# Kernel optimization log

Hardware: AMD Instinct MI355X
Metric: run time of the kernel (lower is better)

## Reference

```python
import jax, jax.numpy as jnp
import numpy as np

B_SZ, SEQ, D_MODEL, D_STATE = 4, 4096, 1024, 16
LN_EPS = 1e-5


def setup_inputs() -> dict:
    key = jax.random.key(0)
    ks = jax.random.split(key, 6)
    x = jax.random.normal(ks[0], (B_SZ, SEQ, D_MODEL), jnp.float32)
    # A_log ~ U(-3, -1) per _init_weights
    A_log = jax.random.uniform(ks[1], (D_MODEL, D_STATE), jnp.float32, -3.0, -1.0)
    # xavier-ish init for projections
    B_w = jax.random.normal(ks[2], (D_STATE, D_MODEL), jnp.float32) / np.sqrt(D_MODEL)
    C_w = jax.random.normal(ks[3], (D_STATE, D_MODEL), jnp.float32) / np.sqrt(D_MODEL)
    D = jnp.ones((D_MODEL,), jnp.float32)
    gate_w = jax.random.normal(ks[4], (D_MODEL, D_MODEL), jnp.float32) / np.sqrt(D_MODEL)
    gate_b = jnp.zeros((D_MODEL,), jnp.float32)
    ln_gamma = jnp.ones((D_MODEL,), jnp.float32)
    ln_beta = jnp.zeros((D_MODEL,), jnp.float32)
    return {"x": x, "A_log": A_log, "B_w": B_w, "C_w": C_w, "D": D,
            "gate_w": gate_w, "gate_b": gate_b,
            "ln_gamma": ln_gamma, "ln_beta": ln_beta}


def reference(x, A_log, B_w, C_w, D, gate_w, gate_b, ln_gamma, ln_beta):
    b, s, d = x.shape
    n = A_log.shape[1]
    A = jnp.exp(A_log)                      # [d, n]
    Bx = jnp.einsum('bsd,nd->bsn', x, B_w)  # input-dependent B_t
    Cx = jnp.einsum('bsd,nd->bsn', x, C_w)  # input-dependent C_t

    def step(h, inp):
        x_t, B_t, C_t = inp                 # [b,d], [b,n], [b,n]
        h = h * A[None] + B_t[:, None, :] * x_t[:, :, None]   # [b,d,n]
        y_t = jnp.einsum('bdn,bn->bd', h, C_t) + D * x_t
        return h, y_t

    h0 = jnp.zeros((b, d, n), x.dtype)
    xs = (jnp.swapaxes(x, 0, 1), jnp.swapaxes(Bx, 0, 1), jnp.swapaxes(Cx, 0, 1))
    _, ys = jax.lax.scan(step, h0, xs)      # ys: [s,b,d]
    y = jnp.swapaxes(ys, 0, 1)              # [b,s,d]

    gate = jax.nn.sigmoid(jnp.einsum('bsd,ed->bse', x, gate_w) + gate_b)
    out = gate * y + (1.0 - gate) * x

    mu = jnp.mean(out, axis=-1, keepdims=True)
    var = jnp.var(out, axis=-1, keepdims=True)
    out = (out - mu) * jax.lax.rsqrt(var + LN_EPS) * ln_gamma + ln_beta
    # dropout is identity in eval mode
    return out
```

## Files before the change

kernel.cpp:

```cpp
#include <hip/hip_runtime.h>

#define B_SZ 4
#define SEQ  4096
#define DM   1024
#define DSTATE 16
#define ROWS (B_SZ*SEQ)

typedef unsigned short u16;
typedef __attribute__((ext_vector_type(8))) short   s16x8;
typedef __attribute__((ext_vector_type(4))) float   f32x4;
typedef __attribute__((ext_vector_type(4))) u16     u16x4;

__device__ inline float bf2f(u16 u) {
    unsigned v = ((unsigned)u) << 16;
    float f; __builtin_memcpy(&f, &v, 4); return f;
}
__device__ inline u16 f2bf(float f) {
    unsigned u; __builtin_memcpy(&u, &f, 4);
    return (u16)((u + 0x7FFFu + ((u >> 16) & 1u)) >> 16);
}
__device__ inline f32x4 mfma16(s16x8 a, s16x8 b, f32x4 c) {
    return __builtin_amdgcn_mfma_f32_16x16x32_bf16(a, b, c, 0, 0, 0);
}
__device__ inline void gl_lds16(const u16* g, u16* l) {
    __builtin_amdgcn_global_load_lds(
        (const __attribute__((address_space(1))) unsigned int*)g,
        (__attribute__((address_space(3))) unsigned int*)l, 16, 0, 0);
}

__global__ __launch_bounds__(256) void k_cvt_w(
    const float* __restrict__ gw, const float* __restrict__ Bw,
    const float* __restrict__ Cw, u16* __restrict__ gwb,
    u16* __restrict__ bwh, u16* __restrict__ bwl,
    u16* __restrict__ cwh, u16* __restrict__ cwl)
{
    int blk = blockIdx.x;
    if (blk < 1024) {
        int i = blk * 256 + threadIdx.x;
        f32x4 v = ((const f32x4*)gw)[i];
        u16x4 o;
#pragma unroll
        for (int c = 0; c < 4; c++) o[c] = f2bf(v[c]);
        ((u16x4*)gwb)[i] = o;
    } else {
        int isC = (blk >= 1040);
        const float* src = isC ? Cw : Bw;
        u16* dh = isC ? cwh : bwh;
        u16* dl = isC ? cwl : bwl;
        int i = (blk - (isC ? 1040 : 1024)) * 256 + threadIdx.x;
        f32x4 v = ((const f32x4*)src)[i];
        u16x4 h, l;
#pragma unroll
        for (int c = 0; c < 4; c++) {
            h[c] = f2bf(v[c]);
            l[c] = f2bf(v[c] - bf2f(h[c]));
        }
        ((u16x4*)dh)[i] = h;
        ((u16x4*)dl)[i] = l;
    }
}

__global__ __launch_bounds__(64) void k_bxcx(
    const float* __restrict__ x,
    const u16* __restrict__ bwh, const u16* __restrict__ bwl,
    const u16* __restrict__ cwh, const u16* __restrict__ cwl,
    u16* __restrict__ xh,
    float* __restrict__ Bx, float* __restrict__ Cx)
{
    int lane = threadIdx.x;
    int lo = lane & 15, hi = lane >> 4;
    int m0 = blockIdx.x * 16;
    f32x4 accB = {}, accC = {};
    for (int k0 = 0; k0 < DM; k0 += 32) {
        size_t woff = (size_t)lo * DM + k0 + hi * 8;
        s16x8 bh = *(const s16x8*)(bwh + woff);
        s16x8 bl = *(const s16x8*)(bwl + woff);
        s16x8 ch = *(const s16x8*)(cwh + woff);
        s16x8 cl = *(const s16x8*)(cwl + woff);
        size_t aoff = (size_t)(m0 + lo) * DM + k0 + hi * 8;
        f32x4 v0 = *(const f32x4*)(x + aoff);
        f32x4 v1 = *(const f32x4*)(x + aoff + 4);
        s16x8 ah, al;
#pragma unroll
        for (int c = 0; c < 4; c++) {
            u16 h0 = f2bf(v0[c]);
            ah[c]     = (short)h0;
            al[c]     = (short)f2bf(v0[c] - bf2f(h0));
            u16 h1 = f2bf(v1[c]);
            ah[4 + c] = (short)h1;
            al[4 + c] = (short)f2bf(v1[c] - bf2f(h1));
        }
        *(s16x8*)(xh + aoff) = ah;
        accB = mfma16(ah, bh, accB);
        accB = mfma16(al, bh, accB);
        accB = mfma16(ah, bl, accB);
        accC = mfma16(ah, ch, accC);
        accC = mfma16(al, ch, accC);
        accC = mfma16(ah, cl, accC);
    }
#pragma unroll
    for (int r = 0; r < 4; r++) {
        int m = m0 + hi * 4 + r;
        Bx[(size_t)m * DSTATE + lo] = accB[r];
        Cx[(size_t)m * DSTATE + lo] = accC[r];
    }
}

#define GBM 256
#define GBN 256
#define GBK 64

__global__ __launch_bounds__(512) void k_gate(
    const u16* __restrict__ xh, const u16* __restrict__ gwb,
    const float* __restrict__ gb, float* __restrict__ gate)
{
    __shared__ u16 sA[2][GBM * GBK];
    __shared__ u16 sB[2][GBN * GBK];
    int tid = threadIdx.x;
    int wv = tid >> 6, lane = tid & 63;
    int lo = lane & 15, hi = lane >> 4;
    int wm = wv >> 2, wn = wv & 3;
    int m0 = blockIdx.x * GBM;
    int n0 = blockIdx.y * GBN;

    int r_in = lane >> 3;
    int p    = lane & 7;
    int c    = p ^ r_in;

    auto stage = [&](int buf, int k0) {
#pragma unroll
        for (int q = 0; q < 4; q++) {
            int r = q * 64 + wv * 8 + r_in;
            size_t goff = (size_t)r * DM + k0 + c * 8;
            gl_lds16(xh  + (size_t)m0 * DM + goff, &sA[buf][(q * 64 + wv * 8) * GBK]);
            gl_lds16(gwb + (size_t)n0 * DM + goff, &sB[buf][(q * 64 + wv * 8) * GBK]);
        }
    };

    f32x4 acc[8][4] = {};

    stage(0, 0);
    asm volatile("s_waitcnt vmcnt(0)" ::: "memory");
    __syncthreads();

    for (int ks = 0; ks < DM / GBK; ks++) {
        int buf = ks & 1;
        if (ks + 1 < DM / GBK) stage(buf ^ 1, (ks + 1) * GBK);
#pragma unroll
        for (int kk = 0; kk < 2; kk++) {
            s16x8 afr[8], bfr[4];
#pragma unroll
            for (int j = 0; j < 4; j++) {
                int rb = wn * 64 + j * 16 + lo;
                int pc = (kk * 4 + hi) ^ (rb & 7);
                bfr[j] = *(const s16x8*)&sB[buf][rb * GBK + pc * 8];
            }
#pragma unroll
            for (int i = 0; i < 8; i++) {
                int ra = wm * 128 + i * 16 + lo;
                int pc = (kk * 4 + hi) ^ (ra & 7);
                afr[i] = *(const s16x8*)&sA[buf][ra * GBK + pc * 8];
            }
#pragma unroll
            for (int i = 0; i < 8; i++)
#pragma unroll
                for (int j = 0; j < 4; j++)
                    acc[i][j] = mfma16(afr[i], bfr[j], acc[i][j]);
        }
        asm volatile("s_waitcnt vmcnt(0)" ::: "memory");
        __syncthreads();
    }

#pragma unroll
    for (int i = 0; i < 8; i++)
#pragma unroll
        for (int r = 0; r < 4; r++) {
            int m = m0 + wm * 128 + i * 16 + hi * 4 + r;
#pragma unroll
            for (int j = 0; j < 4; j++) {
                int n = n0 + wn * 64 + j * 16 + lo;
                float v = acc[i][j][r] + gb[n];
                gate[(size_t)m * DM + n] = 1.0f / (1.0f + __expf(-v));
            }
        }
}

#define CHUNK_L 64
#define LOOKBACK 16

__global__ __launch_bounds__(256) void k_scan(
    const float* __restrict__ x, const float* __restrict__ A_log,
    const float* __restrict__ Bx, const float* __restrict__ Cx,
    const float* __restrict__ Dvec, float* gate_out)
{
    __shared__ float sBx[(CHUNK_L + LOOKBACK) * DSTATE];
    __shared__ float sCx[(CHUNK_L + LOOKBACK) * DSTATE];
    int d = blockIdx.x * 256 + threadIdx.x;
    int b = blockIdx.z;
    int t0 = blockIdx.y * CHUNK_L;
    int tstart = t0 - LOOKBACK; if (tstart < 0) tstart = 0;
    int lb = t0 - tstart;
    int T  = lb + CHUNK_L;
    int NB = T >> 3;
    int nv = T * (DSTATE / 4);

    const f32x4* gBg = (const f32x4*)(Bx + ((size_t)b * SEQ + tstart) * DSTATE);
    const f32x4* gCg = (const f32x4*)(Cx + ((size_t)b * SEQ + tstart) * DSTATE);
    for (int i = threadIdx.x; i < nv; i += 256) {
        ((f32x4*)sBx)[i] = gBg[i];
        ((f32x4*)sCx)[i] = gCg[i];
    }

    float A[DSTATE], h[DSTATE];
    const f32x4* ga = (const f32x4*)(A_log + (size_t)d * DSTATE);
#pragma unroll
    for (int q = 0; q < 4; q++) {
        f32x4 av = ga[q];
#pragma unroll
        for (int c = 0; c < 4; c++) {
            A[q * 4 + c] = expf(av[c]);
            h[q * 4 + c] = 0.0f;
        }
    }
    float Dd = Dvec[d];
    __syncthreads();

    const float* xp = x + ((size_t)b * SEQ + tstart) * DM + d;
    float* gp = gate_out + ((size_t)b * SEQ + t0) * DM + d;

    const f32x4* sB4 = (const f32x4*)sBx;
    const f32x4* sC4 = (const f32x4*)sCx;

    auto pf = [&](int bd, float (&xr)[8], float (&gr)[8]) {
        int base = bd * 8;
#pragma unroll
        for (int q = 0; q < 8; q++) xr[q] = xp[(size_t)(base + q) * DM];
        if (base >= lb) {
#pragma unroll
            for (int q = 0; q < 8; q++) gr[q] = gp[(size_t)(base + q - lb) * DM];
        }
    };

    auto body = [&](int bd, float (&xr)[8], float (&gr)[8]) {
        int base = bd * 8;
        if (base >= lb) {
            float* go = gp + (size_t)(base - lb) * DM;
#pragma unroll
            for (int q = 0; q < 8; q++) {
                int idx = base + q;
                float xv = xr[q], gv = gr[q];
                f32x4 vb0 = sB4[idx * 4 + 0], vb1 = sB4[idx * 4 + 1];
                f32x4 vb2 = sB4[idx * 4 + 2], vb3 = sB4[idx * 4 + 3];
                f32x4 vc0 = sC4[idx * 4 + 0], vc1 = sC4[idx * 4 + 1];
                f32x4 vc2 = sC4[idx * 4 + 2], vc3 = sC4[idx * 4 + 3];
                float y0 = 0.f, y1 = 0.f, y2 = 0.f, y3 = 0.f;
#pragma unroll
                for (int c = 0; c < 4; c++) {
                    h[c]      = h[c]      * A[c]      + vb0[c] * xv;  y0 += h[c]      * vc0[c];
                    h[4 + c]  = h[4 + c]  * A[4 + c]  + vb1[c] * xv;  y1 += h[4 + c]  * vc1[c];
                    h[8 + c]  = h[8 + c]  * A[8 + c]  + vb2[c] * xv;  y2 += h[8 + c]  * vc2[c];
                    h[12 + c] = h[12 + c] * A[12 + c] + vb3[c] * xv;  y3 += h[12 + c] * vc3[c];
                }
                float yv = ((y0 + y1) + (y2 + y3)) + Dd * xv;
                go[(size_t)q * DM] = gv * yv + (1.0f - gv) * xv;
            }
        } else {
#pragma unroll
            for (int q = 0; q < 8; q++) {
                int idx = base + q;
                float xv = xr[q];
                f32x4 vb0 = sB4[idx * 4 + 0], vb1 = sB4[idx * 4 + 1];
                f32x4 vb2 = sB4[idx * 4 + 2], vb3 = sB4[idx * 4 + 3];
#pragma unroll
                for (int c = 0; c < 4; c++) {
                    h[c]      = h[c]      * A[c]      + vb0[c] * xv;
                    h[4 + c]  = h[4 + c]  * A[4 + c]  + vb1[c] * xv;
                    h[8 + c]  = h[8 + c]  * A[8 + c]  + vb2[c] * xv;
                    h[12 + c] = h[12 + c] * A[12 + c] + vb3[c] * xv;
                }
            }
        }
    };

    float xA[8], gA[8], xB[8], gB8[8];
    pf(0, xA, gA);
    for (int bd = 0; bd < NB; bd += 2) {
        pf(bd + 1, xB, gB8);
        body(bd, xA, gA);
        if (bd + 2 < NB) pf(bd + 2, xA, gA);
        body(bd + 1, xB, gB8);
    }
}

__global__ __launch_bounds__(256) void k_ln(
    float* data, const float* __restrict__ gamma, const float* __restrict__ beta)
{
    int wv = threadIdx.x >> 6, lane = threadIdx.x & 63;
    int row = blockIdx.x * 4 + wv;
    f32x4* rp = (f32x4*)(data + (size_t)row * DM);
    f32x4 v[4];
#pragma unroll
    for (int j = 0; j < 4; j++) v[j] = rp[lane + 64 * j];
    float s = 0.0f, s2 = 0.0f;
#pragma unroll
    for (int j = 0; j < 4; j++)
#pragma unroll
        for (int c = 0; c < 4; c++) { float t = v[j][c]; s += t; s2 += t * t; }
#pragma unroll
    for (int off = 32; off > 0; off >>= 1) {
        s  += __shfl_down(s,  off);
        s2 += __shfl_down(s2, off);
    }
    s = __shfl(s, 0); s2 = __shfl(s2, 0);
    float mu  = s  * (1.0f / DM);
    float var = s2 * (1.0f / DM) - mu * mu;
    float rs  = rsqrtf(var + 1e-5f);
#pragma unroll
    for (int j = 0; j < 4; j++) {
        int c0 = (lane + 64 * j) * 4;
        f32x4 o;
#pragma unroll
        for (int c = 0; c < 4; c++)
            o[c] = (v[j][c] - mu) * rs * gamma[c0 + c] + beta[c0 + c];
        rp[lane + 64 * j] = o;
    }
}

extern "C" void kernel_launch(void* const* d_in, const int* in_sizes, int n_in,
                              void* d_out, int out_size, void* d_ws, size_t ws_size,
                              hipStream_t stream)
{
    const float* x     = (const float*)d_in[0];
    const float* A_log = (const float*)d_in[1];
    const float* Bw    = (const float*)d_in[2];
    const float* Cw    = (const float*)d_in[3];
    const float* Dv    = (const float*)d_in[4];
    const float* gw    = (const float*)d_in[5];
    const float* gb    = (const float*)d_in[6];
    const float* gam   = (const float*)d_in[7];
    const float* bet   = (const float*)d_in[8];
    float* out = (float*)d_out;

    char* ws = (char*)d_ws;
    u16*   xh  = (u16*)  ws;
    u16*   gwb = (u16*)  (ws + (64u << 20));
    u16*   bwh = (u16*)  (ws + (66u << 20));
    u16*   bwl = (u16*)  (ws + (66u << 20) + (32u << 10));
    u16*   cwh = (u16*)  (ws + (66u << 20) + (64u << 10));
    u16*   cwl = (u16*)  (ws + (66u << 20) + (96u << 10));
    float* Bx  = (float*)(ws + (67u << 20));
    float* Cx  = (float*)(ws + (68u << 20));

    k_cvt_w<<<1056, 256, 0, stream>>>(gw, Bw, Cw, gwb, bwh, bwl, cwh, cwl);
    k_bxcx<<<ROWS / 16, 64, 0, stream>>>(x, bwh, bwl, cwh, cwl, xh, Bx, Cx);
    k_gate<<<dim3(ROWS / GBM, DM / GBN), 512, 0, stream>>>(xh, gwb, gb, out);
    k_scan<<<dim3(DM / 256, SEQ / CHUNK_L, B_SZ), 256, 0, stream>>>(
        x, A_log, Bx, Cx, Dv, out);
    k_ln<<<ROWS / 4, 256, 0, stream>>>(out, gam, bet);
}
```

Before: 266.2 us.

## Split gate GEMM K-step into four quadrant phases with staggered half-tile prefetch

Restructures the gate GEMM main loop so each 256x256 tile is computed as four 128x128 quadrant phases. The next K-tile's A and B halves are loaded in four separate pieces between phases, using partial vmcnt waits instead of a full drain. Each wave's accumulator layout is changed to cover interleaved quadrants, and MFMA bursts are wrapped in s_setprio to favour math issue. The goal is to hide global-to-LDS load latency behind compute and spread memory traffic more evenly, at the cost of more barriers per K-step and fragile hand-tuned vmcnt counts.

```diff
diff --git a/kernel.cpp b/kernel.cpp
--- a/kernel.cpp
+++ b/kernel.cpp
@@ -27,6 +27,8 @@
         (const __attribute__((address_space(1))) unsigned int*)g,
         (__attribute__((address_space(3))) unsigned int*)l, 16, 0, 0);
 }
+
+#define WAITV(N) asm volatile("s_waitcnt vmcnt(" #N ")" ::: "memory")
 
 __global__ __launch_bounds__(256) void k_cvt_w(
     const float* __restrict__ gw, const float* __restrict__ Bw,
@@ -109,6 +111,7 @@
 #define GBM 256
 #define GBN 256
 #define GBK 64
+#define NKT (DM / GBK)
 
 __global__ __launch_bounds__(512) void k_gate(
     const u16* __restrict__ xh, const u16* __restrict__ gwb,
@@ -127,62 +130,95 @@
     int p    = lane & 7;
     int c    = p ^ r_in;
 
-    auto stage = [&](int buf, int k0) {
-#pragma unroll
-        for (int q = 0; q < 4; q++) {
-            int r = q * 64 + wv * 8 + r_in;
-            size_t goff = (size_t)r * DM + k0 + c * 8;
-            gl_lds16(xh  + (size_t)m0 * DM + goff, &sA[buf][(q * 64 + wv * 8) * GBK]);
-            gl_lds16(gwb + (size_t)n0 * DM + goff, &sB[buf][(q * 64 + wv * 8) * GBK]);
+    auto stage_half = [&](int buf, int kt, int isB, int half) {
+        const u16* src = isB ? (gwb + (size_t)n0 * DM) : (xh + (size_t)m0 * DM);
+        u16* dst = isB ? sB[buf] : sA[buf];
+#pragma unroll
+        for (int q = 0; q < 2; q++) {
+            int rbase = half * 128 + q * 64 + wv * 8;
+            size_t goff = (size_t)(rbase + r_in) * DM + kt * GBK + c * 8;
+            gl_lds16(src + goff, &dst[rbase * GBK]);
         }
     };
 
-    f32x4 acc[8][4] = {};
-
-    stage(0, 0);
-    asm volatile("s_waitcnt vmcnt(0)" ::: "memory");
-    __syncthreads();
-
-    for (int ks = 0; ks < DM / GBK; ks++) {
-        int buf = ks & 1;
-        if (ks + 1 < DM / GBK) stage(buf ^ 1, (ks + 1) * GBK);
-#pragma unroll
-        for (int kk = 0; kk < 2; kk++) {
-            s16x8 afr[8], bfr[4];
-#pragma unroll
-            for (int j = 0; j < 4; j++) {
-                int rb = wn * 64 + j * 16 + lo;
-                int pc = (kk * 4 + hi) ^ (rb & 7);
-                bfr[j] = *(const s16x8*)&sB[buf][rb * GBK + pc * 8];
+    f32x4 acc[2][4][2][2] = {};
+
+#define PHASE(QM, QN)                                                         \
+    do {                                                                      \
+        s16x8 afr[2][4], bfr[2][2];                                           \
+        _Pragma("unroll")                                                     \
+        for (int kk = 0; kk < 2; kk++) {                                      \
+            _Pragma("unroll")                                                 \
+            for (int i2 = 0; i2 < 4; i2++) {                                  \
+                int ra = (QM) * 128 + wm * 64 + i2 * 16 + lo;                 \
+                int pc = (kk * 4 + hi) ^ (ra & 7);                            \
+                afr[kk][i2] = *(const s16x8*)&sA[buf][ra * GBK + pc * 8];     \
+            }                                                                 \
+            _Pragma("unroll")                                                 \
+            for (int j2 = 0; j2 < 2; j2++) {                                  \
+                int rb = (QN) * 128 + wn * 32 + j2 * 16 + lo;                 \
+                int pc = (kk * 4 + hi) ^ (rb & 7);                            \
+                bfr[kk][j2] = *(const s16x8*)&sB[buf][rb * GBK + pc * 8];     \
+            }                                                                 \
+        }                                                                     \
+        __builtin_amdgcn_s_setprio(1);                                        \
+        _Pragma("unroll")                                                     \
+        for (int kk = 0; kk < 2; kk++)                                        \
+            _Pragma("unroll")                                                 \
+            for (int i2 = 0; i2 < 4; i2++)                                    \
+                _Pragma("unroll")                                             \
+                for (int j2 = 0; j2 < 2; j2++)                                \
+                    acc[QM][i2][QN][j2] =                                     \
+                        mfma16(afr[kk][i2], bfr[kk][j2], acc[QM][i2][QN][j2]);\
+        __builtin_amdgcn_s_setprio(0);                                        \
+    } while (0)
+
+    stage_half(0, 0, 0, 0);
+    stage_half(0, 0, 1, 0);
+    stage_half(0, 0, 1, 1);
+    stage_half(0, 0, 0, 1);
+
+    for (int t = 0; t < NKT; t++) {
+        int buf = t & 1;
+        int hasN = (t + 1 < NKT);
+        if (hasN) { stage_half(buf ^ 1, t + 1, 0, 0); WAITV(6); }
+        else      { WAITV(4); }
+        __builtin_amdgcn_s_barrier();
+        PHASE(0, 0);
+        __builtin_amdgcn_s_barrier();
+        if (hasN) { stage_half(buf ^ 1, t + 1, 1, 0); WAITV(6); }
+        else      { WAITV(2); }
+        __builtin_amdgcn_s_barrier();
+        PHASE(0, 1);
+        __builtin_amdgcn_s_barrier();
+        if (hasN) { stage_half(buf ^ 1, t + 1, 1, 1); WAITV(6); }
+        else      { WAITV(0); }
+        __builtin_amdgcn_s_barrier();
+        PHASE(1, 0);
+        __builtin_amdgcn_s_barrier();
+        if (hasN) stage_half(buf ^ 1, t + 1, 0, 1);
+        __builtin_amdgcn_s_barrier();
+        PHASE(1, 1);
+        __builtin_amdgcn_s_barrier();
+    }
+#undef PHASE
+
+#pragma unroll
+    for (int qm = 0; qm < 2; qm++)
+#pragma unroll
+        for (int i = 0; i < 4; i++)
+#pragma unroll
+            for (int r = 0; r < 4; r++) {
+                int m = m0 + qm * 128 + wm * 64 + i * 16 + hi * 4 + r;
+#pragma unroll
+                for (int qn = 0; qn < 2; qn++)
+#pragma unroll
+                    for (int j = 0; j < 2; j++) {
+                        int n = n0 + qn * 128 + wn * 32 + j * 16 + lo;
+                        float v = acc[qm][i][qn][j][r] + gb[n];
+                        gate[(size_t)m * DM + n] = 1.0f / (1.0f + __expf(-v));
+                    }
             }
-#pragma unroll
-            for (int i = 0; i < 8; i++) {
-                int ra = wm * 128 + i * 16 + lo;
-                int pc = (kk * 4 + hi) ^ (ra & 7);
-                afr[i] = *(const s16x8*)&sA[buf][ra * GBK + pc * 8];
-            }
-#pragma unroll
-            for (int i = 0; i < 8; i++)
-#pragma unroll
-                for (int j = 0; j < 4; j++)
-                    acc[i][j] = mfma16(afr[i], bfr[j], acc[i][j]);
-        }
-        asm volatile("s_waitcnt vmcnt(0)" ::: "memory");
-        __syncthreads();
-    }
-
-#pragma unroll
-    for (int i = 0; i < 8; i++)
-#pragma unroll
-        for (int r = 0; r < 4; r++) {
-            int m = m0 + wm * 128 + i * 16 + hi * 4 + r;
-#pragma unroll
-            for (int j = 0; j < 4; j++) {
-                int n = n0 + wn * 64 + j * 16 + lo;
-                float v = acc[i][j][r] + gb[n];
-                gate[(size_t)m * DM + n] = 1.0f / (1.0f + __expf(-v));
-            }
-        }
 }
 
 #define CHUNK_L 64
```

Result: no change. 269.4 us (+1.2%).
